# Kernel tuning notes

Measured on AMD Instinct MI355X. Metric: run time of the kernel, lower is better.

## Reference

```python
import jax, jax.numpy as jnp
import numpy as np

PC_RANGE = (-50.0, -50.0, -4.0, 50.0, 50.0, 4.0)
IMG_H, IMG_W = 256.0, 704.0
EPS = 1e-5


def _bilinear_sample(feat, u, v):
    # feat [H,W,C]; u,v [M] in [0,1]; matches F.grid_sample(align_corners=False, padding_mode='zeros')
    H, W, _ = feat.shape
    x = u * W - 0.5
    y = v * H - 0.5
    x0 = jnp.floor(x)
    y0 = jnp.floor(y)
    dx = (x - x0)[:, None]
    dy = (y - y0)[:, None]
    x0 = x0.astype(jnp.int32)
    y0 = y0.astype(jnp.int32)

    def g(xi, yi):
        inb = ((xi >= 0) & (xi < W) & (yi >= 0) & (yi < H)).astype(feat.dtype)[:, None]
        return feat[jnp.clip(yi, 0, H - 1), jnp.clip(xi, 0, W - 1)] * inb

    return (g(x0, y0) * (1 - dx) * (1 - dy) + g(x0 + 1, y0) * dx * (1 - dy)
            + g(x0, y0 + 1) * (1 - dx) * dy + g(x0 + 1, y0 + 1) * dx * dy)


def _conv1x1(t, w, b):
    return jnp.einsum('bchw,oc->bohw', t, w) + b[None, :, None, None]


def _inorm(t, eps=1e-5):
    # InstanceNorm2d (affine=False): normalize per (b, c) over spatial dims
    m = t.mean(axis=(2, 3), keepdims=True)
    var = t.var(axis=(2, 3), keepdims=True)
    return (t - m) * jax.lax.rsqrt(var + eps)


def _forward(feat, lidar2img, bev_pos, pe_w1, pe_b1, pe_w2, pe_b2, pe_w3, pe_b3,
             c1_w, c1_b, c2_w, c2_b, c3_w, c3_b):
    B, N, C, Hf, Wf = feat.shape
    _, P, Hb, Wb, _ = bev_pos.shape
    Q = Hb * Wb
    lo = jnp.asarray(PC_RANGE[:3], feat.dtype)
    hi = jnp.asarray(PC_RANGE[3:], feat.dtype)
    # 'b p h w d -> b (h w) p d', then scale normalized coords into pc_range
    ref01 = jnp.transpose(bev_pos, (0, 2, 3, 1, 4)).reshape(B, Q, P, 3)
    ref = ref01 * (hi - lo) + lo
    # project through per-camera lidar2img (homogeneous)
    pts = jnp.concatenate([ref, jnp.ones_like(ref[..., :1])], axis=-1)  # [B,Q,P,4]
    cam = jnp.einsum('bnij,bqpj->bnqpi', lidar2img, pts)                # [B,N,Q,P,4]
    homo = cam[..., 2]
    z = jnp.maximum(homo, EPS)
    u = cam[..., 0] / z / IMG_W
    v = cam[..., 1] / z / IMG_H
    valid = ((homo > EPS) & (u > 0.0) & (u < 1.0) & (v > 0.0) & (v < 1.0)).astype(feat.dtype)
    # bilinear gather per camera; feats to channel-last ('b n (g c) h w -> (b g) n h w c', G=1)
    fmap = jnp.transpose(feat, (0, 1, 3, 4, 2)).reshape(B * N, Hf, Wf, C)
    samp = jax.vmap(_bilinear_sample)(fmap, u.reshape(B * N, Q * P), v.reshape(B * N, Q * P))
    samp = samp.reshape(B, N, Q, P, C) * valid[..., None]
    samp = samp.sum(axis=1)  # sum over cameras -> [B,Q,P,C]
    # PositionalEncodingMap(3 -> 256 -> 256 -> 128) on normalized reference points
    pe = jax.nn.relu(ref01 @ pe_w1 + pe_b1)
    pe = jax.nn.relu(pe @ pe_w2 + pe_b2)
    pe = pe @ pe_w3 + pe_b3
    samp = samp + pe
    # 'b (h w) g p c -> b (p g c) h w' with g=1
    x = jnp.transpose(samp.reshape(B, Hb, Wb, P, C), (0, 3, 4, 1, 2)).reshape(B, P * C, Hb, Wb)
    gelu = lambda t: jax.nn.gelu(t, approximate=False)
    x = gelu(_inorm(_conv1x1(x, c1_w, c1_b)))
    x = gelu(_inorm(_conv1x1(x, c2_w, c2_b)))
    x = _conv1x1(x, c3_w, c3_b)
    return x


def setup_inputs() -> dict:
    key = jax.random.key(0)
    ks = jax.random.split(key, 16)
    B, N, C, Hf, Wf = 1, 6, 128, 32, 88
    P, Hb, Wb = 4, 160, 160
    E = 128
    MID = 256
    s = 0.02
    return {
        'feat': jax.random.normal(ks[0], (B, N, C, Hf, Wf), jnp.float32),
        'lidar2img': jax.random.normal(ks[1], (B, N, 4, 4), jnp.float32),
        'bev_pos': jax.random.uniform(ks[2], (B, P, Hb, Wb, 3), jnp.float32),
        'pe_w1': jax.random.normal(ks[3], (3, MID), jnp.float32) * s,
        'pe_b1': jnp.zeros((MID,), jnp.float32),
        'pe_w2': jax.random.normal(ks[4], (MID, MID), jnp.float32) * s,
        'pe_b2': jnp.zeros((MID,), jnp.float32),
        'pe_w3': jax.random.normal(ks[5], (MID, E), jnp.float32) * s,
        'pe_b3': jnp.zeros((E,), jnp.float32),
        'c1_w': jax.random.normal(ks[6], (4 * E, P * 128), jnp.float32) * s,
        'c1_b': jnp.zeros((4 * E,), jnp.float32),
        'c2_w': jax.random.normal(ks[7], (E, 4 * E), jnp.float32) * s,
        'c2_b': jnp.zeros((E,), jnp.float32),
        'c3_w': jax.random.normal(ks[8], (E, E), jnp.float32) * s,
        'c3_b': jnp.zeros((E,), jnp.float32),
    }


def reference(feat, lidar2img, bev_pos, pe_w1, pe_b1, pe_w2, pe_b2, pe_w3, pe_b3,
              c1_w, c1_b, c2_w, c2_b, c3_w, c3_b):
    return _forward(feat, lidar2img, bev_pos, pe_w1, pe_b1, pe_w2, pe_b2, pe_w3, pe_b3,
                    c1_w, c1_b, c2_w, c2_b, c3_w, c3_b)
```

## Files before the change

kernel.cpp:

```cpp
#include <hip/hip_runtime.h>
#include <cstdint>
#include <cstddef>

using frag8 = __attribute__((ext_vector_type(8))) short;
using f32x4 = __attribute__((ext_vector_type(4))) float;

__device__ __forceinline__ float b2f_bits(unsigned short u) {
    union { uint32_t u32; float f; } x; x.u32 = ((uint32_t)u) << 16; return x.f;
}
__device__ __forceinline__ float b2f_lo(uint32_t pk) {
    return __builtin_bit_cast(float, pk << 16);
}
__device__ __forceinline__ float b2f_hi(uint32_t pk) {
    return __builtin_bit_cast(float, pk & 0xffff0000u);
}
__device__ __forceinline__ unsigned short f2b(float f) {
    uint32_t u = __builtin_bit_cast(uint32_t, f);
    uint32_t r = (u + 0x7fffu + ((u >> 16) & 1u)) >> 16;
    return (unsigned short)r;
}

#define HF 32
#define WFEAT 88
#define NCAM 6
#define NPT 102400
#define BM 128
#define BN 128
#define BK 64

__global__ __launch_bounds__(256) void k_prep(const float* __restrict__ feat,
                                              const float* __restrict__ pw2,
                                              const float* __restrict__ pw3,
                                              const float* __restrict__ c1w,
                                              const float* __restrict__ c2w,
                                              const float* __restrict__ c3w,
                                              const float* __restrict__ pw1,
                                              const float* __restrict__ pb1,
                                              const float* __restrict__ l2i,
                                              const float* __restrict__ bev,
                                              unsigned short* __restrict__ featT,
                                              unsigned short* __restrict__ W2Tb,
                                              unsigned short* __restrict__ W3Tb,
                                              unsigned short* __restrict__ C1Wb,
                                              unsigned short* __restrict__ C2Wb,
                                              unsigned short* __restrict__ C3Wb,
                                              unsigned short* __restrict__ H1,
                                              float* __restrict__ stats,
                                              int* __restrict__ poff,
                                              float4* __restrict__ pwts) {
    __shared__ unsigned short tile[64 * 132];
    int b = blockIdx.x, t = threadIdx.x;
    if (b < 25600) {
        int idx = b * 256 + t;
        int m = idx >> 6;
        int o4 = (idx & 63) * 4;
        int q = m >> 2, p = m & 3;
        int h = q / 160, w = q - h * 160;
        const float* bv = bev + ((p * 160 + h) * 160 + w) * 3;
        float cx = bv[0], cy = bv[1], cz = bv[2];
        float4 a0 = *(const float4*)(pw1 + o4);
        float4 a1 = *(const float4*)(pw1 + 256 + o4);
        float4 a2 = *(const float4*)(pw1 + 512 + o4);
        float4 bb = *(const float4*)(pb1 + o4);
        ushort4 o;
        o.x = f2b(fmaxf(cx * a0.x + cy * a1.x + cz * a2.x + bb.x, 0.f));
        o.y = f2b(fmaxf(cx * a0.y + cy * a1.y + cz * a2.y + bb.y, 0.f));
        o.z = f2b(fmaxf(cx * a0.z + cy * a1.z + cz * a2.z + bb.z, 0.f));
        o.w = f2b(fmaxf(cx * a0.w + cy * a1.w + cz * a2.w + bb.w, 0.f));
        *(ushort4*)(H1 + (size_t)m * 256 + o4) = o;
        return;
    }
    b -= 25600;
    if (b < 2400) {
        int idx = b * 256 + t;
        int n = idx / NPT, pt = idx - n * NPT;
        int q = pt >> 2, p = pt & 3;
        int h = q / 160, w = q - h * 160;
        const float* bv = bev + ((p * 160 + h) * 160 + w) * 3;
        float rx = bv[0] * 100.f - 50.f;
        float ry = bv[1] * 100.f - 50.f;
        float rz = bv[2] * 8.f - 4.f;
        const float* M = l2i + n * 16;
        float c0   = M[0] * rx + M[1] * ry + M[2]  * rz + M[3];
        float c1v  = M[4] * rx + M[5] * ry + M[6]  * rz + M[7];
        float homo = M[8] * rx + M[9] * ry + M[10] * rz + M[11];
        float z = fmaxf(homo, 1e-5f);
        float u = c0 / z / 704.0f;
        float v = c1v / z / 256.0f;
        if (!(homo > 1e-5f && u > 0.f && u < 1.f && v > 0.f && v < 1.f)) {
            poff[idx] = -1;
            return;
        }
        float fx = u * (float)WFEAT - 0.5f;
        float fy = v * (float)HF - 0.5f;
        float fx0 = floorf(fx), fy0 = floorf(fy);
        float dx = fx - fx0, dy = fy - fy0;
        int x0 = (int)fx0, y0 = (int)fy0;
        float wxa = (x0 < 0) ? dx : 1.f - dx;
        float wxb = (x0 >= 0 && x0 < WFEAT - 1) ? dx : 0.f;
        float wya = (y0 < 0) ? dy : 1.f - dy;
        float wyb = (y0 >= 0 && y0 < HF - 1) ? dy : 0.f;
        int bx = max(x0, 0), by = max(y0, 0);
        poff[idx] = ((n * HF + by) * WFEAT + bx) << 7;
        pwts[idx] = make_float4(wxa * wya, wxb * wya, wxa * wyb, wxb * wyb);
        return;
    }
    b -= 2400;
    if (b < 264) {
        int n = b / 44;
        int s0 = (b - n * 44) * 64;
        #pragma unroll
        for (int i = 0; i < 32; ++i) {
            int e = i * 256 + t;
            int c = e >> 6, sl = e & 63;
            tile[sl * 132 + c] = f2b(feat[(size_t)(n * 128 + c) * 2816 + s0 + sl]);
        }
        __syncthreads();
        #pragma unroll
        for (int j = 0; j < 8; ++j) {
            int flat = j * 1024 + t * 4;
            int sl = flat >> 7, c = flat & 127;
            ushort4 v = *(const ushort4*)(tile + sl * 132 + c);
            *(ushort4*)(featT + (size_t)(n * 2816 + s0 + sl) * 128 + c) = v;
        }
        return;
    }
    b -= 264;
    if (b < 256) {
        int idx = b * 256 + t;
        int r = idx >> 8, c = idx & 255;
        W2Tb[c * 256 + r] = f2b(pw2[idx]);
        return;
    }
    b -= 256;
    if (b < 128) {
        int idx = b * 256 + t;
        int r = idx >> 7, c = idx & 127;
        W3Tb[c * 128 + 0] = W3Tb[c * 128];
        W3Tb[c * 256 + r] = f2b(pw3[idx]);
        return;
    }
    b -= 128;
    if (b < 1024) { int idx = b * 256 + t; C1Wb[idx] = f2b(c1w[idx]); return; }
    b -= 1024;
    if (b < 256)  { int idx = b * 256 + t; C2Wb[idx] = f2b(c2w[idx]); return; }
    b -= 256;
    if (b < 64)   { int idx = b * 256 + t; C3Wb[idx] = f2b(c3w[idx]); return; }
    #pragma unroll
    for (int j = 0; j < 10; ++j) stats[t * 10 + j] = 0.f;
}

__global__ __launch_bounds__(256) void k_sample2(const unsigned short* __restrict__ featT,
                                                 const int* __restrict__ poff,
                                                 const float4* __restrict__ pwts,
                                                 unsigned short* __restrict__ samp) {
    int pt = blockIdx.x * 4 + (threadIdx.x >> 6);
    int lane = threadIdx.x & 63;
    int c2 = lane * 2;
    int offs[NCAM];
    float4 ww[NCAM];
    #pragma unroll
    for (int n = 0; n < NCAM; ++n) offs[n] = poff[n * NPT + pt];
    #pragma unroll
    for (int n = 0; n < NCAM; ++n) ww[n] = pwts[n * NPT + pt];
    float acc0 = 0.f, acc1 = 0.f;
    #pragma unroll
    for (int n = 0; n < NCAM; ++n) {
        if (offs[n] >= 0) {
            const unsigned short* base = featT + offs[n] + c2;
            uint32_t p00 = *(const uint32_t*)(base);
            uint32_t p01 = *(const uint32_t*)(base + 128);
            uint32_t p10 = *(const uint32_t*)(base + WFEAT * 128);
            uint32_t p11 = *(const uint32_t*)(base + WFEAT * 128 + 128);
            float4 w = ww[n];
            acc0 += w.x * b2f_lo(p00) + w.y * b2f_lo(p01) + w.z * b2f_lo(p10) + w.w * b2f_lo(p11);
            acc1 += w.x * b2f_hi(p00) + w.y * b2f_hi(p01) + w.z * b2f_hi(p10) + w.w * b2f_hi(p11);
        }
    }
    uint32_t outpk = (uint32_t)f2b(acc0) | ((uint32_t)f2b(acc1) << 16);
    *(uint32_t*)(samp + (size_t)pt * 128 + c2) = outpk;
}

__device__ __forceinline__ void stage_tile_big(const unsigned short* __restrict__ g, int ld,
                                               unsigned short* lds, int t) {
    int r = t >> 2, cs = t & 3;
    int cl = cs ^ ((r >> 1) & 3);
    __builtin_amdgcn_global_load_lds(
        (const __attribute__((address_space(1))) void*)(g + (size_t)r * ld + cl * 8),
        (__attribute__((address_space(3))) void*)(lds + (t >> 6) * 512),
        16, 0, 0);
}

__device__ __forceinline__ frag8 frag_read_big(const unsigned short* lds, int row, int chunk) {
    return *(const frag8*)(lds + row * 32 + ((chunk ^ ((row >> 1) & 3)) << 3));
}

__device__ __forceinline__ void mma_tile_big(const unsigned short* As, const unsigned short* Bs,
                                             int wm, int wn, int lane, f32x4 (&acc)[4][4]) {
    int lm = lane & 15, lq = lane >> 4;
    frag8 a[4], b[4];
    #pragma unroll
    for (int t = 0; t < 4; ++t) a[t] = frag_read_big(As, wm * 64 + t * 16 + lm, lq);
    #pragma unroll
    for (int t = 0; t < 4; ++t) b[t] = frag_read_big(Bs, wn * 64 + t * 16 + lm, lq);
    #pragma unroll
    for (int tm = 0; tm < 4; ++tm)
        #pragma unroll
        for (int tn = 0; tn < 4; ++tn)
            acc[tm][tn] = __builtin_amdgcn_mfma_f32_16x16x32_bf16(a[tm], b[tn], acc[tm][tn], 0, 0, 0);
}

template <int KT>
__device__ __forceinline__ void gemm_loop_big(const unsigned short* __restrict__ A, int ldA,
                                              const unsigned short* __restrict__ B, int ldB,
                                              unsigned short (*As)[256 * 32],
                                              unsigned short (*Bs)[256 * 32],
                                              int t, int wm, int wn, int lane,
                                              f32x4 (&acc)[4][4]) {
    stage_tile_big(A, ldA, As[0], t);
    stage_tile_big(B, ldB, Bs[0], t);
    __syncthreads();
    #pragma unroll
    for (int kt = 0; kt < KT; ++kt) {
        int cur = kt & 1, nxt = cur ^ 1;
        if (kt + 1 < KT) {
            stage_tile_big(A + (kt + 1) * 32, ldA, As[nxt], t);
            stage_tile_big(B + (kt + 1) * 32, ldB, Bs[nxt], t);
        }
        mma_tile_big(As[cur], Bs[cur], wm, wn, lane, acc);
        __syncthreads();
    }
}

__global__ __launch_bounds__(1024) void k_gemm_pe2_big(const unsigned short* __restrict__ A,
                                                       const unsigned short* __restrict__ Bt,
                                                       const float* __restrict__ bias,
                                                       unsigned short* __restrict__ H2) {
    __shared__ unsigned short As[2][256 * 32], Bs[2][256 * 32];
    int t = threadIdx.x, lane = t & 63, wid = t >> 6;
    int wm = wid >> 2, wn = wid & 3;
    int m0 = blockIdx.x * 256;
    f32x4 acc[4][4] = {};
    gemm_loop_big<8>(A + (size_t)m0 * 256, 256, Bt, 256, As, Bs, t, wm, wn, lane, acc);
    int lm = lane & 15, lq = lane >> 4;
    #pragma unroll
    for (int tn = 0; tn < 4; ++tn) {
        int n = wn * 64 + tn * 16 + lm;
        float bn = bias[n];
        #pragma unroll
        for (int tm = 0; tm < 4; ++tm) {
            int mb = m0 + wm * 64 + tm * 16 + lq * 4;
            #pragma unroll
            for (int rr = 0; rr < 4; ++rr)
                H2[(size_t)(mb + rr) * 256 + n] = f2b(fmaxf(acc[tm][tn][rr] + bn, 0.f));
        }
    }
}

__global__ __launch_bounds__(1024) void k_gemm_conv1_big(const unsigned short* __restrict__ A,
                                                         const unsigned short* __restrict__ Bt,
                                                         const float* __restrict__ bias,
                                                         unsigned short* __restrict__ Y,
                                                         float* __restrict__ st) {
    __shared__ unsigned short As[2][256 * 32], Bs[2][256 * 32];
    int t = threadIdx.x, lane = t & 63, wid = t >> 6;
    int wm = wid >> 2, wn = wid & 3;
    int m0 = blockIdx.x * 256, n0 = blockIdx.y * 256;
    f32x4 acc[4][4] = {};
    gemm_loop_big<16>(A + (size_t)m0 * 512, 512, Bt + (size_t)n0 * 512, 512,
                      As, Bs, t, wm, wn, lane, acc);
    int lm = lane & 15, lq = lane >> 4;
    #pragma unroll
    for (int tn = 0; tn < 4; ++tn) {
        int n = n0 + wn * 64 + tn * 16 + lm;
        float bn = bias[n];
        float s1 = 0.f, s2 = 0.f;
        #pragma unroll
        for (int tm = 0; tm < 4; ++tm) {
            int mb = m0 + wm * 64 + tm * 16 + lq * 4;
            #pragma unroll
            for (int rr = 0; rr < 4; ++rr) {
                float v = acc[tm][tn][rr] + bn;
                Y[(size_t)(mb + rr) * 512 + n] = f2b(v);
                s1 += v; s2 += v * v;
            }
        }
        s1 += __shfl_xor(s1, 16); s1 += __shfl_xor(s1, 32);
        s2 += __shfl_xor(s2, 16); s2 += __shfl_xor(s2, 32);
        if (lq == 0) { atomicAdd(&st[n], s1); atomicAdd(&st[512 + n], s2); }
    }
}

__device__ __forceinline__ void stage_tile(const unsigned short* __restrict__ g, int ld,
                                           unsigned short* lds, int wave, int lane) {
    #pragma unroll
    for (int j = 0; j < 4; ++j) {
        int idx = wave * 256 + j * 64 + lane;
        int r = idx >> 3;
        int cs = idx & 7;
        int cl = cs ^ (r & 7);
        __builtin_amdgcn_global_load_lds(
            (const __attribute__((address_space(1))) void*)(g + (size_t)r * ld + cl * 8),
            (__attribute__((address_space(3))) void*)(lds + wave * 2048 + j * 512),
            16, 0, 0);
    }
}

__device__ __forceinline__ frag8 frag_read(const unsigned short* lds, int row, int chunk) {
    return *(const frag8*)(lds + row * 64 + ((chunk ^ (row & 7)) << 3));
}

__device__ __forceinline__ void mma_tile(const unsigned short* As, const unsigned short* Bs,
                                         int wm, int wn, int lane, f32x4 (&acc)[4][4]) {
    int lm = lane & 15, lq = lane >> 4;
    #pragma unroll
    for (int kk = 0; kk < 2; ++kk) {
        frag8 a[4], b[4];
        #pragma unroll
        for (int t = 0; t < 4; ++t) a[t] = frag_read(As, wm * 64 + t * 16 + lm, kk * 4 + lq);
        #pragma unroll
        for (int t = 0; t < 4; ++t) b[t] = frag_read(Bs, wn * 64 + t * 16 + lm, kk * 4 + lq);
        #pragma unroll
        for (int tm = 0; tm < 4; ++tm)
            #pragma unroll
            for (int tn = 0; tn < 4; ++tn)
                acc[tm][tn] = __builtin_amdgcn_mfma_f32_16x16x32_bf16(a[tm], b[tn], acc[tm][tn], 0, 0, 0);
    }
}

__global__ __launch_bounds__(256) void k_gemm_pe3(const unsigned short* __restrict__ A,
                                                  const unsigned short* __restrict__ Bt,
                                                  const float* __restrict__ bias,
                                                  const unsigned short* __restrict__ samp,
                                                  unsigned short* __restrict__ X) {
    __shared__ unsigned short As[BM * BK], Bs[BN * BK];
    int lane = threadIdx.x & 63, wave = threadIdx.x >> 6;
    int wm = wave >> 1, wn = wave & 1;
    int m0 = blockIdx.x * BM;
    f32x4 acc[4][4] = {};
    for (int kt = 0; kt < 4; ++kt) {
        stage_tile(A + (size_t)m0 * 256 + kt * BK, 256, As, wave, lane);
        stage_tile(Bt + (size_t)kt * BK, 256, Bs, wave, lane);
        __syncthreads();
        mma_tile(As, Bs, wm, wn, lane, acc);
        __syncthreads();
    }
    int lm = lane & 15, lq = lane >> 4;
    #pragma unroll
    for (int tn = 0; tn < 4; ++tn) {
        int n = wn * 64 + tn * 16 + lm;
        float bn = bias[n];
        #pragma unroll
        for (int tm = 0; tm < 4; ++tm) {
            int mb = m0 + wm * 64 + tm * 16 + lq * 4;
            #pragma unroll
            for (int rr = 0; rr < 4; ++rr) {
                size_t off = (size_t)(mb + rr) * 128 + n;
                X[off] = f2b(acc[tm][tn][rr] + bn + b2f_bits(samp[off]));
            }
        }
    }
}

template <int K, bool STATS>
__global__ __launch_bounds__(256) void k_gemm_conv(const unsigned short* __restrict__ A,
                                                   const unsigned short* __restrict__ Bt,
                                                   const float* __restrict__ bias,
                                                   unsigned short* __restrict__ Y, int ldY,
                                                   float* __restrict__ st, int C) {
    __shared__ unsigned short As[BM * BK], Bs[BN * BK];
    int lane = threadIdx.x & 63, wave = threadIdx.x >> 6;
    int wm = wave >> 1, wn = wave & 1;
    int m0 = blockIdx.x * BM, n0 = blockIdx.y * BN;
    f32x4 acc[4][4] = {};
    for (int kt = 0; kt < K / BK; ++kt) {
        stage_tile(A + (size_t)m0 * K + kt * BK, K, As, wave, lane);
        stage_tile(Bt + (size_t)n0 * K + kt * BK, K, Bs, wave, lane);
        __syncthreads();
        mma_tile(As, Bs, wm, wn, lane, acc);
        __syncthreads();
    }
    int lm = lane & 15, lq = lane >> 4;
    #pragma unroll
    for (int tn = 0; tn < 4; ++tn) {
        int n = n0 + wn * 64 + tn * 16 + lm;
        float bn = bias[n];
        float s1 = 0.f, s2 = 0.f;
        #pragma unroll
        for (int tm = 0; tm < 4; ++tm) {
            int mb = m0 + wm * 64 + tm * 16 + lq * 4;
            #pragma unroll
            for (int rr = 0; rr < 4; ++rr) {
                float v = acc[tm][tn][rr] + bn;
                Y[(size_t)(mb + rr) * ldY + n] = f2b(v);
                if (STATS) { s1 += v; s2 += v * v; }
            }
        }
        if (STATS) {
            s1 += __shfl_xor(s1, 16); s1 += __shfl_xor(s1, 32);
            s2 += __shfl_xor(s2, 16); s2 += __shfl_xor(s2, 32);
            if (lq == 0) { atomicAdd(&st[n], s1); atomicAdd(&st[C + n], s2); }
        }
    }
}

__global__ __launch_bounds__(256) void k_gemm_conv3(const unsigned short* __restrict__ A,
                                                    const unsigned short* __restrict__ Bt,
                                                    const float* __restrict__ bias,
                                                    float* __restrict__ out) {
    __shared__ unsigned short As[BM * BK], Bs[BN * BK];
    int lane = threadIdx.x & 63, wave = threadIdx.x >> 6;
    int wm = wave >> 1, wn = wave & 1;
    int m0 = blockIdx.x * BM;
    f32x4 acc[4][4] = {};
    for (int kt = 0; kt < 2; ++kt) {
        stage_tile(A + (size_t)m0 * 128 + kt * BK, 128, As, wave, lane);
        stage_tile(Bt + (size_t)kt * BK, 128, Bs, wave, lane);
        __syncthreads();
        mma_tile(As, Bs, wm, wn, lane, acc);
        __syncthreads();
    }
    int lm = lane & 15, lq = lane >> 4;
    #pragma unroll
    for (int tn = 0; tn < 4; ++tn) {
        int n = wn * 64 + tn * 16 + lm;
        float bn = bias[n];
        #pragma unroll
        for (int tm = 0; tm < 4; ++tm) {
            int mb = m0 + wm * 64 + tm * 16 + lq * 4;
            float4 pk;
            pk.x = acc[tm][tn][0] + bn;
            pk.y = acc[tm][tn][1] + bn;
            pk.z = acc[tm][tn][2] + bn;
            pk.w = acc[tm][tn][3] + bn;
            *(float4*)(out + (size_t)n * 25600 + mb) = pk;
        }
    }
}

__global__ void k_normgelu8f(const unsigned short* __restrict__ Y, const float* __restrict__ st,
                             unsigned short* __restrict__ X2, int Cmask, int C, float inv_n,
                             int total8) {
    int i8 = blockIdx.x * 256 + threadIdx.x;
    if (i8 >= total8) return;
    int e0 = i8 * 8;
    int c = e0 & Cmask;
    uint4 y = *(const uint4*)(Y + e0);
    float4 s1a = *(const float4*)(st + c);
    float4 s1b = *(const float4*)(st + c + 4);
    float4 s2a = *(const float4*)(st + C + c);
    float4 s2b = *(const float4*)(st + C + c + 4);
    float mu[8] = { s1a.x * inv_n, s1a.y * inv_n, s1a.z * inv_n, s1a.w * inv_n,
                    s1b.x * inv_n, s1b.y * inv_n, s1b.z * inv_n, s1b.w * inv_n };
    float sq[8] = { s2a.x, s2a.y, s2a.z, s2a.w, s2b.x, s2b.y, s2b.z, s2b.w };
    float rs[8];
    #pragma unroll
    for (int j = 0; j < 8; ++j) rs[j] = rsqrtf(sq[j] * inv_n - mu[j] * mu[j] + 1e-5f);
    const float is2 = 0.70710678118654752f;
    unsigned int yw[4] = {y.x, y.y, y.z, y.w};
    unsigned int ow[4];
    #pragma unroll
    for (int j = 0; j < 4; ++j) {
        float v0 = (b2f_bits((unsigned short)(yw[j] & 0xffffu)) - mu[j * 2]) * rs[j * 2];
        float v1 = (b2f_bits((unsigned short)(yw[j] >> 16)) - mu[j * 2 + 1]) * rs[j * 2 + 1];
        float g0 = 0.5f * v0 * (1.f + erff(v0 * is2));
        float g1 = 0.5f * v1 * (1.f + erff(v1 * is2));
        ow[j] = (uint32_t)f2b(g0) | ((uint32_t)f2b(g1) << 16);
    }
    *(uint4*)(X2 + e0) = make_uint4(ow[0], ow[1], ow[2], ow[3]);
}

extern "C" void kernel_launch(void* const* d_in, const int* in_sizes, int n_in,
                              void* d_out, int out_size, void* d_ws, size_t ws_size,
                              hipStream_t stream) {
    (void)in_sizes; (void)n_in; (void)out_size; (void)ws_size;
    const float* feat = (const float*)d_in[0];
    const float* l2i  = (const float*)d_in[1];
    const float* bev  = (const float*)d_in[2];
    const float* pw1  = (const float*)d_in[3];
    const float* pb1  = (const float*)d_in[4];
    const float* pw2  = (const float*)d_in[5];
    const float* pb2  = (const float*)d_in[6];
    const float* pw3  = (const float*)d_in[7];
    const float* pb3  = (const float*)d_in[8];
    const float* c1w  = (const float*)d_in[9];
    const float* c1b  = (const float*)d_in[10];
    const float* c2w  = (const float*)d_in[11];
    const float* c2b  = (const float*)d_in[12];
    const float* c3w  = (const float*)d_in[13];
    const float* c3b  = (const float*)d_in[14];
    float* outp = (float*)d_out;
    char* ws = (char*)d_ws;

    unsigned short* featT = (unsigned short*)(ws + 0);
    unsigned short* W2Tb  = (unsigned short*)(ws + 4348416);
    unsigned short* W3Tb  = (unsigned short*)(ws + 4479488);
    unsigned short* C1Wb  = (unsigned short*)(ws + 4545024);
    unsigned short* C2Wb  = (unsigned short*)(ws + 5069312);
    unsigned short* C3Wb  = (unsigned short*)(ws + 5200384);
    float* stats          = (float*)(ws + 5233152);
    int*    poff          = (int*)(ws + 5247488);
    float4* pwts          = (float4*)(ws + 7705088);
    char* BUF1 = ws + 17535488;
    char* BUF2 = ws + 69964288;
    char* BUF3 = ws + 122393088;

    float* st512 = stats;
    float* st128 = stats + 2048;

    unsigned short* H1   = (unsigned short*)BUF1;
    unsigned short* H2   = (unsigned short*)BUF2;
    unsigned short* samp = (unsigned short*)BUF3;
    unsigned short* X    = (unsigned short*)BUF1;
    unsigned short* Y1   = (unsigned short*)BUF2;
    unsigned short* X2   = (unsigned short*)BUF3;
    unsigned short* Y2   = (unsigned short*)BUF1;
    unsigned short* X3   = (unsigned short*)(BUF1 + 6553600);

    k_prep<<<29993, 256, 0, stream>>>(feat, pw2, pw3, c1w, c2w, c3w, pw1, pb1, l2i, bev,
                                      featT, W2Tb, W3Tb, C1Wb, C2Wb, C3Wb, H1, stats,
                                      poff, pwts);

    k_sample2<<<25600, 256, 0, stream>>>(featT, poff, pwts, samp);

    k_gemm_pe2_big<<<400, 1024, 0, stream>>>(H1, W2Tb, pb2, H2);
    k_gemm_pe3<<<dim3(800, 1), 256, 0, stream>>>(H2, W3Tb, pb3, samp, X);

    k_gemm_conv1_big<<<dim3(100, 2), 1024, 0, stream>>>(X, C1Wb, c1b, Y1, st512);
    k_normgelu8f<<<6400, 256, 0, stream>>>(Y1, st512, X2, 511, 512, 1.f / 25600.f, 1638400);

    k_gemm_conv<512, true><<<dim3(200, 1), 256, 0, stream>>>(X2, C2Wb, c2b, Y2, 128, st128, 128);
    k_normgelu8f<<<1600, 256, 0, stream>>>(Y2, st128, X3, 127, 128, 1.f / 25600.f, 409600);

    k_gemm_conv3<<<dim3(200, 1), 256, 0, stream>>>(X3, C3Wb, c3b, outp);
}
```

Baseline: 277.5 us.

## Fuse PE layer-1 into PE layer-2 GEMM and drop big-tile GEMM kernels

Computes the first positional-encoding layer (3->256 linear + ReLU) on the fly inside the PE layer-2 GEMM, building A fragments in registers from bev coordinates and weights held in LDS. This removes the H1 intermediate buffer, with its global write and read, and shrinks the prep launch. The 1024-thread big-tile GEMMs for PE2 and conv1 are replaced with the generic 128x128 kernel (conv1 now uses k_gemm_conv on a 200x4 grid). The cost is that each of the two N-tiles recomputes layer 1, and the per-fragment conversion to bf16 adds ALU work inside the MFMA loop.

```diff
diff --git a/kernel.cpp b/kernel.cpp
--- a/kernel.cpp
+++ b/kernel.cpp
@@ -34,8 +34,6 @@
                                               const float* __restrict__ c1w,
                                               const float* __restrict__ c2w,
                                               const float* __restrict__ c3w,
-                                              const float* __restrict__ pw1,
-                                              const float* __restrict__ pb1,
                                               const float* __restrict__ l2i,
                                               const float* __restrict__ bev,
                                               unsigned short* __restrict__ featT,
@@ -44,33 +42,11 @@
                                               unsigned short* __restrict__ C1Wb,
                                               unsigned short* __restrict__ C2Wb,
                                               unsigned short* __restrict__ C3Wb,
-                                              unsigned short* __restrict__ H1,
                                               float* __restrict__ stats,
                                               int* __restrict__ poff,
                                               float4* __restrict__ pwts) {
     __shared__ unsigned short tile[64 * 132];
     int b = blockIdx.x, t = threadIdx.x;
-    if (b < 25600) {
-        int idx = b * 256 + t;
-        int m = idx >> 6;
-        int o4 = (idx & 63) * 4;
-        int q = m >> 2, p = m & 3;
-        int h = q / 160, w = q - h * 160;
-        const float* bv = bev + ((p * 160 + h) * 160 + w) * 3;
-        float cx = bv[0], cy = bv[1], cz = bv[2];
-        float4 a0 = *(const float4*)(pw1 + o4);
-        float4 a1 = *(const float4*)(pw1 + 256 + o4);
-        float4 a2 = *(const float4*)(pw1 + 512 + o4);
-        float4 bb = *(const float4*)(pb1 + o4);
-        ushort4 o;
-        o.x = f2b(fmaxf(cx * a0.x + cy * a1.x + cz * a2.x + bb.x, 0.f));
-        o.y = f2b(fmaxf(cx * a0.y + cy * a1.y + cz * a2.y + bb.y, 0.f));
-        o.z = f2b(fmaxf(cx * a0.z + cy * a1.z + cz * a2.z + bb.z, 0.f));
-        o.w = f2b(fmaxf(cx * a0.w + cy * a1.w + cz * a2.w + bb.w, 0.f));
-        *(ushort4*)(H1 + (size_t)m * 256 + o4) = o;
-        return;
-    }
-    b -= 25600;
     if (b < 2400) {
         int idx = b * 256 + t;
         int n = idx / NPT, pt = idx - n * NPT;
@@ -136,7 +112,6 @@
     if (b < 128) {
         int idx = b * 256 + t;
         int r = idx >> 7, c = idx & 127;
-        W3Tb[c * 128 + 0] = W3Tb[c * 128];
         W3Tb[c * 256 + r] = f2b(pw3[idx]);
         return;
     }
@@ -181,116 +156,6 @@
     *(uint32_t*)(samp + (size_t)pt * 128 + c2) = outpk;
 }
 
-__device__ __forceinline__ void stage_tile_big(const unsigned short* __restrict__ g, int ld,
-                                               unsigned short* lds, int t) {
-    int r = t >> 2, cs = t & 3;
-    int cl = cs ^ ((r >> 1) & 3);
-    __builtin_amdgcn_global_load_lds(
-        (const __attribute__((address_space(1))) void*)(g + (size_t)r * ld + cl * 8),
-        (__attribute__((address_space(3))) void*)(lds + (t >> 6) * 512),
-        16, 0, 0);
-}
-
-__device__ __forceinline__ frag8 frag_read_big(const unsigned short* lds, int row, int chunk) {
-    return *(const frag8*)(lds + row * 32 + ((chunk ^ ((row >> 1) & 3)) << 3));
-}
-
-__device__ __forceinline__ void mma_tile_big(const unsigned short* As, const unsigned short* Bs,
-                                             int wm, int wn, int lane, f32x4 (&acc)[4][4]) {
-    int lm = lane & 15, lq = lane >> 4;
-    frag8 a[4], b[4];
-    #pragma unroll
-    for (int t = 0; t < 4; ++t) a[t] = frag_read_big(As, wm * 64 + t * 16 + lm, lq);
-    #pragma unroll
-    for (int t = 0; t < 4; ++t) b[t] = frag_read_big(Bs, wn * 64 + t * 16 + lm, lq);
-    #pragma unroll
-    for (int tm = 0; tm < 4; ++tm)
-        #pragma unroll
-        for (int tn = 0; tn < 4; ++tn)
-            acc[tm][tn] = __builtin_amdgcn_mfma_f32_16x16x32_bf16(a[tm], b[tn], acc[tm][tn], 0, 0, 0);
-}
-
-template <int KT>
-__device__ __forceinline__ void gemm_loop_big(const unsigned short* __restrict__ A, int ldA,
-                                              const unsigned short* __restrict__ B, int ldB,
-                                              unsigned short (*As)[256 * 32],
-                                              unsigned short (*Bs)[256 * 32],
-                                              int t, int wm, int wn, int lane,
-                                              f32x4 (&acc)[4][4]) {
-    stage_tile_big(A, ldA, As[0], t);
-    stage_tile_big(B, ldB, Bs[0], t);
-    __syncthreads();
-    #pragma unroll
-    for (int kt = 0; kt < KT; ++kt) {
-        int cur = kt & 1, nxt = cur ^ 1;
-        if (kt + 1 < KT) {
-            stage_tile_big(A + (kt + 1) * 32, ldA, As[nxt], t);
-            stage_tile_big(B + (kt + 1) * 32, ldB, Bs[nxt], t);
-        }
-        mma_tile_big(As[cur], Bs[cur], wm, wn, lane, acc);
-        __syncthreads();
-    }
-}
-
-__global__ __launch_bounds__(1024) void k_gemm_pe2_big(const unsigned short* __restrict__ A,
-                                                       const unsigned short* __restrict__ Bt,
-                                                       const float* __restrict__ bias,
-                                                       unsigned short* __restrict__ H2) {
-    __shared__ unsigned short As[2][256 * 32], Bs[2][256 * 32];
-    int t = threadIdx.x, lane = t & 63, wid = t >> 6;
-    int wm = wid >> 2, wn = wid & 3;
-    int m0 = blockIdx.x * 256;
-    f32x4 acc[4][4] = {};
-    gemm_loop_big<8>(A + (size_t)m0 * 256, 256, Bt, 256, As, Bs, t, wm, wn, lane, acc);
-    int lm = lane & 15, lq = lane >> 4;
-    #pragma unroll
-    for (int tn = 0; tn < 4; ++tn) {
-        int n = wn * 64 + tn * 16 + lm;
-        float bn = bias[n];
-        #pragma unroll
-        for (int tm = 0; tm < 4; ++tm) {
-            int mb = m0 + wm * 64 + tm * 16 + lq * 4;
-            #pragma unroll
-            for (int rr = 0; rr < 4; ++rr)
-                H2[(size_t)(mb + rr) * 256 + n] = f2b(fmaxf(acc[tm][tn][rr] + bn, 0.f));
-        }
-    }
-}
-
-__global__ __launch_bounds__(1024) void k_gemm_conv1_big(const unsigned short* __restrict__ A,
-                                                         const unsigned short* __restrict__ Bt,
-                                                         const float* __restrict__ bias,
-                                                         unsigned short* __restrict__ Y,
-                                                         float* __restrict__ st) {
-    __shared__ unsigned short As[2][256 * 32], Bs[2][256 * 32];
-    int t = threadIdx.x, lane = t & 63, wid = t >> 6;
-    int wm = wid >> 2, wn = wid & 3;
-    int m0 = blockIdx.x * 256, n0 = blockIdx.y * 256;
-    f32x4 acc[4][4] = {};
-    gemm_loop_big<16>(A + (size_t)m0 * 512, 512, Bt + (size_t)n0 * 512, 512,
-                      As, Bs, t, wm, wn, lane, acc);
-    int lm = lane & 15, lq = lane >> 4;
-    #pragma unroll
-    for (int tn = 0; tn < 4; ++tn) {
-        int n = n0 + wn * 64 + tn * 16 + lm;
-        float bn = bias[n];
-        float s1 = 0.f, s2 = 0.f;
-        #pragma unroll
-        for (int tm = 0; tm < 4; ++tm) {
-            int mb = m0 + wm * 64 + tm * 16 + lq * 4;
-            #pragma unroll
-            for (int rr = 0; rr < 4; ++rr) {
-                float v = acc[tm][tn][rr] + bn;
-                Y[(size_t)(mb + rr) * 512 + n] = f2b(v);
-                s1 += v; s2 += v * v;
-            }
-        }
-        s1 += __shfl_xor(s1, 16); s1 += __shfl_xor(s1, 32);
-        s2 += __shfl_xor(s2, 16); s2 += __shfl_xor(s2, 32);
-        if (lq == 0) { atomicAdd(&st[n], s1); atomicAdd(&st[512 + n], s2); }
-    }
-}
-
 __device__ __forceinline__ void stage_tile(const unsigned short* __restrict__ g, int ld,
                                            unsigned short* lds, int wave, int lane) {
     #pragma unroll
@@ -325,6 +190,88 @@
             #pragma unroll
             for (int tn = 0; tn < 4; ++tn)
                 acc[tm][tn] = __builtin_amdgcn_mfma_f32_16x16x32_bf16(a[tm], b[tn], acc[tm][tn], 0, 0, 0);
+    }
+}
+
+__global__ __launch_bounds__(256) void k_pe12(const float* __restrict__ bev,
+                                              const float* __restrict__ pw1,
+                                              const float* __restrict__ pb1,
+                                              const unsigned short* __restrict__ Bt,
+                                              const float* __restrict__ bias,
+                                              unsigned short* __restrict__ H2) {
+    __shared__ unsigned short Bs[BN * BK];
+    __shared__ __align__(16) float wls[4 * 256];
+    __shared__ float bevs[3 * 128];
+    int t = threadIdx.x, lane = t & 63, wave = t >> 6;
+    int wm = wave >> 1, wn = wave & 1;
+    int m0 = blockIdx.x * BM, n0 = blockIdx.y * BN;
+    {
+        int i = t * 4;
+        int j = i >> 8, c = i & 255;
+        float4 v = (j < 3) ? *(const float4*)(pw1 + j * 256 + c)
+                           : *(const float4*)(pb1 + c);
+        *(float4*)(wls + i) = v;
+    }
+    if (t < 128) {
+        int m = m0 + t;
+        int q = m >> 2, p = m & 3;
+        int h = q / 160, w = q - h * 160;
+        const float* bv = bev + ((size_t)((p * 160 + h) * 160 + w)) * 3;
+        bevs[t] = bv[0]; bevs[128 + t] = bv[1]; bevs[256 + t] = bv[2];
+    }
+    __syncthreads();
+    int lm = lane & 15, lq = lane >> 4;
+    float rx[4], ry[4], rz[4];
+    #pragma unroll
+    for (int tm = 0; tm < 4; ++tm) {
+        int r = wm * 64 + tm * 16 + lm;
+        rx[tm] = bevs[r]; ry[tm] = bevs[128 + r]; rz[tm] = bevs[256 + r];
+    }
+    f32x4 acc[4][4] = {};
+    for (int kt = 0; kt < 4; ++kt) {
+        stage_tile(Bt + (size_t)n0 * 256 + kt * BK, 256, Bs, wave, lane);
+        __syncthreads();
+        #pragma unroll
+        for (int kk = 0; kk < 2; ++kk) {
+            int ch = kk * 4 + lq;
+            int kc = kt * 64 + ch * 8;
+            float4 a0l = *(const float4*)(wls + kc),       a0h = *(const float4*)(wls + kc + 4);
+            float4 a1l = *(const float4*)(wls + 256 + kc), a1h = *(const float4*)(wls + 256 + kc + 4);
+            float4 a2l = *(const float4*)(wls + 512 + kc), a2h = *(const float4*)(wls + 512 + kc + 4);
+            float4 bbl = *(const float4*)(wls + 768 + kc), bbh = *(const float4*)(wls + 768 + kc + 4);
+            frag8 b[4];
+            #pragma unroll
+            for (int tn = 0; tn < 4; ++tn) b[tn] = frag_read(Bs, wn * 64 + tn * 16 + lm, ch);
+            #pragma unroll
+            for (int tm = 0; tm < 4; ++tm) {
+                float x = rx[tm], y = ry[tm], z = rz[tm];
+                frag8 a;
+                a[0] = (short)f2b(fmaxf(x * a0l.x + y * a1l.x + z * a2l.x + bbl.x, 0.f));
+                a[1] = (short)f2b(fmaxf(x * a0l.y + y * a1l.y + z * a2l.y + bbl.y, 0.f));
+                a[2] = (short)f2b(fmaxf(x * a0l.z + y * a1l.z + z * a2l.z + bbl.z, 0.f));
+                a[3] = (short)f2b(fmaxf(x * a0l.w + y * a1l.w + z * a2l.w + bbl.w, 0.f));
+                a[4] = (short)f2b(fmaxf(x * a0h.x + y * a1h.x + z * a2h.x + bbh.x, 0.f));
+                a[5] = (short)f2b(fmaxf(x * a0h.y + y * a1h.y + z * a2h.y + bbh.y, 0.f));
+                a[6] = (short)f2b(fmaxf(x * a0h.z + y * a1h.z + z * a2h.z + bbh.z, 0.f));
+                a[7] = (short)f2b(fmaxf(x * a0h.w + y * a1h.w + z * a2h.w + bbh.w, 0.f));
+                #pragma unroll
+                for (int tn = 0; tn < 4; ++tn)
+                    acc[tm][tn] = __builtin_amdgcn_mfma_f32_16x16x32_bf16(a, b[tn], acc[tm][tn], 0, 0, 0);
+            }
+        }
+        __syncthreads();
+    }
+    #pragma unroll
+    for (int tn = 0; tn < 4; ++tn) {
+        int n = n0 + wn * 64 + tn * 16 + lm;
+        float bn = bias[n];
+        #pragma unroll
+        for (int tm = 0; tm < 4; ++tm) {
+            int mb = m0 + wm * 64 + tm * 16 + lq * 4;
+            #pragma unroll
+            for (int rr = 0; rr < 4; ++rr)
+                H2[(size_t)(mb + rr) * 256 + n] = f2b(fmaxf(acc[tm][tn][rr] + bn, 0.f));
+        }
     }
 }
 
@@ -508,7 +455,6 @@
     float* st512 = stats;
     float* st128 = stats + 2048;
 
-    unsigned short* H1   = (unsigned short*)BUF1;
     unsigned short* H2   = (unsigned short*)BUF2;
     unsigned short* samp = (unsigned short*)BUF3;
     unsigned short* X    = (unsigned short*)BUF1;
@@ -517,16 +463,16 @@
     unsigned short* Y2   = (unsigned short*)BUF1;
     unsigned short* X3   = (unsigned short*)(BUF1 + 6553600);
 
-    k_prep<<<29993, 256, 0, stream>>>(feat, pw2, pw3, c1w, c2w, c3w, pw1, pb1, l2i, bev,
-                                      featT, W2Tb, W3Tb, C1Wb, C2Wb, C3Wb, H1, stats,
-                                      poff, pwts);
+    k_prep<<<4393, 256, 0, stream>>>(feat, pw2, pw3, c1w, c2w, c3w, l2i, bev,
+                                     featT, W2Tb, W3Tb, C1Wb, C2Wb, C3Wb, stats,
+                                     poff, pwts);
 
     k_sample2<<<25600, 256, 0, stream>>>(featT, poff, pwts, samp);
 
-    k_gemm_pe2_big<<<400, 1024, 0, stream>>>(H1, W2Tb, pb2, H2);
+    k_pe12<<<dim3(800, 2), 256, 0, stream>>>(bev, pw1, pb1, W2Tb, pb2, H2);
     k_gemm_pe3<<<dim3(800, 1), 256, 0, stream>>>(H2, W3Tb, pb3, samp, X);
 
-    k_gemm_conv1_big<<<dim3(100, 2), 1024, 0, stream>>>(X, C1Wb, c1b, Y1, st512);
+    k_gemm_conv<512, true><<<dim3(200, 4), 256, 0, stream>>>(X, C1Wb, c1b, Y1, 512, st512, 512);
     k_normgelu8f<<<6400, 256, 0, stream>>>(Y1, st512, X2, 511, 512, 1.f / 25600.f, 1638400);
 
     k_gemm_conv<512, true><<<dim3(200, 1), 256, 0, stream>>>(X2, C2Wb, c2b, Y2, 128, st128, 128);
```

After: 284.5 us. +2.5%, slower.
